# Kernel optimization log

Measured on AMD Instinct MI355X. Metric: run time of the kernel, lower is better.

Reference implementation:

```python
import math
import jax, jax.numpy as jnp
import numpy as np

N_HEADS = 8
N_POINTS = 4


def bilinear_sample(img, gx, gy):
    """torch F.grid_sample(bilinear, align_corners=True, padding='zeros').
    img: [N,C,H,W]; gx,gy: [N,P] normalized coords (gx -> width axis, gy -> height axis).
    Returns [N,C,P]."""
    N, C, H, W = img.shape
    ix = (gx + 1.0) * 0.5 * (W - 1)
    iy = (gy + 1.0) * 0.5 * (H - 1)
    x0 = jnp.floor(ix); y0 = jnp.floor(iy)
    x1 = x0 + 1.0;      y1 = y0 + 1.0

    def corner(yc, xc, w):
        m = (xc >= 0) & (xc <= W - 1) & (yc >= 0) & (yc <= H - 1)
        xi = jnp.clip(xc, 0, W - 1).astype(jnp.int32)
        yi = jnp.clip(yc, 0, H - 1).astype(jnp.int32)
        v = jax.vmap(lambda im, y, x: im[:, y, x])(img, yi, xi)  # [N,C,P]
        return v * (w * m)[:, None, :]

    return (corner(y0, x0, (x1 - ix) * (y1 - iy))
            + corner(y0, x1, (ix - x0) * (y1 - iy))
            + corner(y1, x0, (x1 - ix) * (iy - y0))
            + corner(y1, x1, (ix - x0) * (iy - y0)))


def forward(query, points, features, cam_M, cam_b, W_off, b_off,
            W_q, b_q, W_k, b_k, W_v, b_v, W_o, b_o):
    B, K, C = query.shape
    ncam = features.shape[0]
    H, W = features.shape[-2:]
    nh, npnt = N_HEADS, N_POINTS
    hd = C // nh
    HW = jnp.asarray([H, W], dtype=query.dtype)

    # camera model: pixel = sigmoid(points @ M^T + b) * [H, W]   -> [ncam,B,K,2]
    px = jax.nn.sigmoid(jnp.einsum('bkj,cij->cbki', points, cam_M)
                        + cam_b[:, None, None, :]) * HW

    # ---- step 1: sample raw features at projected points (per camera) ----
    # original normalizes coord0 by H and coord1 by W (coord0 is grid_sample's x/width axis)
    gx1 = 2.0 * px[..., 0] / H - 1.0          # [ncam,B,K]
    gy1 = 2.0 * px[..., 1] / W - 1.0
    camf = jax.vmap(bilinear_sample)(features, gx1, gy1)   # [ncam,B,C,K]
    camf = jnp.transpose(camf, (1, 3, 0, 2))               # [B,K,ncam,C]

    query_ = query[:, :, None, :] + camf                   # [B,K,ncam,C]
    offsets = (query_ @ W_off.T + b_off).reshape(B, K, ncam, nh, npnt, 2)

    # ---- 1x1 conv key/value projections ----
    kf = (jnp.einsum('cbdhw,ed->cbehw', features, W_k)
          + b_k[None, None, :, None, None]).reshape(ncam, B * nh, hd, H, W)
    vf = (jnp.einsum('cbdhw,ed->cbehw', features, W_v)
          + b_v[None, None, :, None, None]).reshape(ncam, B * nh, hd, H, W)

    # ---- sampling locations with offsets ----
    off = jnp.moveaxis(offsets, 2, 0) / HW                 # [ncam,B,K,nh,np,2]
    pc = px[:, :, :, None, None, :] + off                  # [ncam,B,K,nh,np,2]
    gx = 2.0 * (pc[..., 0] / H) - 1.0
    gy = 2.0 * (pc[..., 1] / W) - 1.0
    # [ncam,B,K,nh,np] -> [ncam, B*nh, K*np]
    gx = jnp.transpose(gx, (0, 1, 3, 2, 4)).reshape(ncam, B * nh, K * npnt)
    gy = jnp.transpose(gy, (0, 1, 3, 2, 4)).reshape(ncam, B * nh, K * npnt)

    keys = jax.vmap(bilinear_sample)(kf, gx, gy)           # [ncam,B*nh,hd,K*np]
    vals = jax.vmap(bilinear_sample)(vf, gx, gy)

    def rearr(t):  # -> [B, nh, K, ncam*np, hd]
        t = t.reshape(ncam, B, nh, hd, K, npnt)
        return jnp.transpose(t, (1, 2, 4, 0, 5, 3)).reshape(B, nh, K, ncam * npnt, hd)

    keys, vals = rearr(keys), rearr(vals)

    q = (query @ W_q.T + b_q).reshape(B, K, nh, hd).transpose(0, 2, 1, 3)  # [B,nh,K,hd]
    logits = jnp.einsum('bhkd,bhkld->bhkl', q, keys) / math.sqrt(hd)
    attn = jax.nn.softmax(logits, axis=-1)
    weighted = jnp.einsum('bhkl,bhkld->bhkd', attn, vals)  # [B,nh,K,hd]
    # faithful to original torch `.view(B, K, embed_dim)` on a [B,nh,K,hd] tensor
    weighted = weighted.reshape(B, K, C)
    return weighted @ W_o.T + b_o


def setup_inputs() -> dict:
    key = jax.random.key(0)
    ks = jax.random.split(key, 16)
    B, K, C = 8, 900, 256
    ncam, H, W = 6, 32, 88
    f = lambda i, shape, s=1.0: jax.random.normal(ks[i], shape, dtype=jnp.float32) * s
    return {
        'query': f(0, (B, K, C)),
        'points': f(1, (B, K, 3)),
        'features': f(2, (ncam, B, C, H, W)),
        'cam_M': f(3, (ncam, 2, 3), 0.5),
        'cam_b': f(4, (ncam, 2), 0.5),
        'W_off': f(5, (2 * N_HEADS * N_POINTS, C), 0.02),
        'b_off': f(6, (2 * N_HEADS * N_POINTS,), 1.0),
        'W_q': f(7, (C, C), 0.02), 'b_q': f(8, (C,), 0.02),
        'W_k': f(9, (C, C), 0.02), 'b_k': f(10, (C,), 0.02),
        'W_v': f(11, (C, C), 0.02), 'b_v': f(12, (C,), 0.02),
        'W_o': f(13, (C, C), 0.02), 'b_o': f(14, (C,), 0.02),
    }


def reference(query, points, features, cam_M, cam_b, W_off, b_off,
              W_q, b_q, W_k, b_k, W_v, b_v, W_o, b_o):
    return forward(query, points, features, cam_M, cam_b, W_off, b_off,
                   W_q, b_q, W_k, b_k, W_v, b_v, W_o, b_o)
```

## Files before the change

kernel.cpp:

```cpp
#include <hip/hip_runtime.h>

typedef __attribute__((ext_vector_type(4))) float f32x4;
typedef __attribute__((ext_vector_type(8))) short bf16x8;
typedef __attribute__((ext_vector_type(4))) unsigned int u32x4;

__device__ __forceinline__ unsigned short f2bf(float f) {
    union { float f; unsigned int u; } x; x.f = f;
    unsigned int u = x.u;
    return (unsigned short)((u + 0x7FFFu + ((u >> 16) & 1u)) >> 16);
}
__device__ __forceinline__ float bf2f(unsigned short b) {
    union { unsigned int u; float f; } x; x.u = ((unsigned int)b) << 16;
    return x.f;
}
__device__ __forceinline__ float u2f(unsigned int u) {
    union { unsigned int u; float f; } x; x.u = u; return x.f;
}


__global__ void prep_wkv(const float* __restrict__ Wk, const float* __restrict__ bk,
                         const float* __restrict__ Wv, const float* __restrict__ bv,
                         unsigned short* __restrict__ Wkv, float* __restrict__ bkv) {
    int i = blockIdx.x * 256 + threadIdx.x;
    if (i < 512 * 256) {
        int n = i >> 8, k = i & 255;
        float v = (n < 256) ? Wk[i] : Wv[i - 65536];
        Wkv[((size_t)(n >> 7) * 8 + (k >> 5)) * 4096 + (n & 127) * 32 + (k & 31)] = f2bf(v);
    }
    if (i < 512) bkv[i] = (i < 256) ? bk[i] : bv[i - 256];
}

__global__ void prep_woff(const float* __restrict__ Woff, unsigned short* __restrict__ Woffp) {
    int n = blockIdx.x, k = threadIdx.x;
    Woffp[(size_t)(k >> 5) * 4096 + n * 32 + (k & 31)] = f2bf(Woff[n * 256 + k]);
}

__global__ __launch_bounds__(256) void transpose_feat(const float* __restrict__ src,
                                                      unsigned short* __restrict__ dst) {
    __shared__ float tile[32][33];
    int img = blockIdx.z;
    int p0 = blockIdx.x * 32;
    int d0 = blockIdx.y * 32;
    int tx = threadIdx.x & 31, ty = threadIdx.x >> 5;
    const float* s = src + (size_t)img * 256 * 2816;
#pragma unroll
    for (int i = 0; i < 4; i++) tile[ty + 8 * i][tx] = s[(size_t)(d0 + ty + 8 * i) * 2816 + p0 + tx];
    __syncthreads();
    int m = img * 2816 + p0;
    unsigned short* o = dst + ((size_t)(m >> 7) * 8 + (d0 >> 5)) * 4096 + (m & 127) * 32;
#pragma unroll
    for (int i = 0; i < 4; i++) o[(ty + 8 * i) * 32 + tx] = f2bf(tile[tx][ty + 8 * i]);
}

__global__ __launch_bounds__(256) void gemm_kv2(
    const unsigned short* __restrict__ A,
    const unsigned short* __restrict__ Wkv,
    const unsigned short* __restrict__ Woffp,
    const float* __restrict__ bias,
    unsigned short* __restrict__ C,
    float* __restrict__ Foff) {
    __shared__ __align__(16) unsigned short Bl[8192];
    __shared__ __align__(16) unsigned short Ar[3][4096];

    const int tid = threadIdx.x, lane = tid & 63, w = tid >> 6;
    const int lrow = lane & 15, lk = lane >> 4;
    const int lsw = (lane >> 2) * 32 + (((lane & 3) ^ ((lane >> 3) & 3)) * 8);
    const int ckx = ((lrow >> 1) & 3);
    const int bid = blockIdx.x;
    const int wgid = (bid & 7) * 1188 + (bid >> 3);
    const int chunk = wgid / 9, bn = wgid % 9;

    const unsigned short* A0 = A + (size_t)chunk * 32768;
    const unsigned short* Bb = (bn < 8)
        ? Wkv + (size_t)(bn >> 1) * 32768 + (bn & 1) * 2048
        : Woffp;
    const int wof = w * 1024;

#define STAGE_B(HALF)                                                                        \
    {                                                                                        \
        _Pragma("unroll")                                                                    \
        for (int i = 0; i < 4; ++i) {                                                        \
            __builtin_amdgcn_global_load_lds(                                                \
                (const __attribute__((address_space(1))) unsigned int*)(Bb + ((HALF) * 4 + w) * 4096 + i * 512 + lsw), \
                (__attribute__((address_space(3))) unsigned int*)&Bl[w * 2048 + i * 512], 16, 0, 0);                   \
        }                                                                                    \
    }

#define STAGE_STEP(S)                                                                        \
    {                                                                                        \
        __builtin_amdgcn_global_load_lds(                                                    \
            (const __attribute__((address_space(1))) unsigned int*)(A0 + (S) * 4096 + wof + lsw),        \
            (__attribute__((address_space(3))) unsigned int*)&Ar[(S) % 3][wof], 16, 0, 0);   \
        __builtin_amdgcn_global_load_lds(                                                    \
            (const __attribute__((address_space(1))) unsigned int*)(A0 + (S) * 4096 + wof + 512 + lsw),  \
            (__attribute__((address_space(3))) unsigned int*)&Ar[(S) % 3][wof + 512], 16, 0, 0);         \
    }

    STAGE_B(0)
    STAGE_STEP(0) STAGE_STEP(1)
    __syncthreads();

    f32x4 acc[2][4] = {};

#define COMP_STEP(S, NW)                                                                     \
    {                                                                                        \
        asm volatile("s_waitcnt vmcnt(%0)" :: "i"(NW) : "memory");                           \
        bf16x8 bfr[4], af[2];                                                                \
        _Pragma("unroll") for (int j = 0; j < 4; ++j)                                        \
            bfr[j] = *(const bf16x8*)&Bl[((S) & 3) * 2048 + (j * 16 + lrow) * 32 + (lk ^ ckx) * 8]; \
        _Pragma("unroll") for (int i = 0; i < 2; ++i)                                        \
            af[i] = *(const bf16x8*)&Ar[(S) % 3][wof + i * 512 + lrow * 32 + (lk ^ ckx) * 8];\
        if ((S) + 2 < 8) {                                                                   \
            asm volatile("s_waitcnt lgkmcnt(0)" ::: "memory");                               \
            STAGE_STEP((S) + 2)                                                              \
        }                                                                                    \
        _Pragma("unroll") for (int i = 0; i < 2; ++i)                                        \
            _Pragma("unroll") for (int j = 0; j < 4; ++j)                                    \
                acc[i][j] = __builtin_amdgcn_mfma_f32_16x16x32_bf16(af[i], bfr[j], acc[i][j], 0, 0, 0); \
    }

    COMP_STEP(0, 4) COMP_STEP(1, 2) COMP_STEP(2, 2) COMP_STEP(3, 2)
    __syncthreads();
    STAGE_B(1)
    __syncthreads();
    COMP_STEP(4, 4) COMP_STEP(5, 2) COMP_STEP(6, 2) COMP_STEP(7, 0)
#undef COMP_STEP
#undef STAGE_STEP
#undef STAGE_B

    if (bn < 8) {
        unsigned short* Cl = &Ar[0][0];
        __syncthreads();
#pragma unroll
        for (int j = 0; j < 4; ++j) {
            float bs = bias[bn * 64 + j * 16 + lrow];
#pragma unroll
            for (int i = 0; i < 2; ++i)
#pragma unroll
                for (int jj = 0; jj < 4; ++jj)
                    Cl[(w * 32 + i * 16 + lk * 4 + jj) * 64 + j * 16 + lrow] =
                        f2bf(acc[i][j][jj] + bs);
        }
        __syncthreads();
#pragma unroll
        for (int it = 0; it < 4; ++it) {
            int idx = it * 256 + tid;
            int row = idx >> 3, col8 = idx & 7;
            int dstcol = (bn < 4)
                ? (bn * 2 + (col8 >> 2)) * 64 + (col8 & 3) * 8
                : ((bn - 4) * 2 + (col8 >> 2)) * 64 + 32 + (col8 & 3) * 8;
            *(f32x4*)(C + (size_t)(chunk * 128 + row) * 512 + dstcol) =
                *(const f32x4*)&Cl[row * 64 + col8 * 8];
        }
    } else {
#pragma unroll
        for (int i = 0; i < 2; ++i)
#pragma unroll
            for (int j = 0; j < 4; ++j)
#pragma unroll
                for (int jj = 0; jj < 4; ++jj) {
                    int m = chunk * 128 + w * 32 + i * 16 + lk * 4 + jj;
                    Foff[(size_t)m * 64 + j * 16 + lrow] = acc[i][j][jj];
                }
    }
}

__global__ __launch_bounds__(384) void sample_offs(
    const float* __restrict__ points, const float* __restrict__ camM,
    const float* __restrict__ camb, const float* __restrict__ Foff,
    const float* __restrict__ qWoff,
    float* __restrict__ offs, float* __restrict__ pxy) {
    int bk = blockIdx.x;
    int b = bk / 900;
    int cam = threadIdx.x >> 6, j = threadIdx.x & 63;
    int cid = cam * 7200 + bk;

    float p0 = points[(size_t)bk * 3 + 0];
    float p1 = points[(size_t)bk * 3 + 1];
    float p2 = points[(size_t)bk * 3 + 2];
    const float* M = camM + cam * 6;
    float s0 = M[0] * p0 + M[1] * p1 + M[2] * p2 + camb[cam * 2 + 0];
    float s1 = M[3] * p0 + M[4] * p1 + M[5] * p2 + camb[cam * 2 + 1];
    float px0 = (1.f / (1.f + expf(-s0))) * 32.f;
    float px1 = (1.f / (1.f + expf(-s1))) * 88.f;
    float gx = 2.f * px0 / 32.f - 1.f, gy = 2.f * px1 / 88.f - 1.f;
    float ix = (gx + 1.f) * 0.5f * 87.f;
    float iy = (gy + 1.f) * 0.5f * 31.f;
    float x0 = floorf(ix), y0 = floorf(iy), x1 = x0 + 1.f, y1 = y0 + 1.f;
    float wx1 = ix - x0, wx0 = x1 - ix, wy1 = iy - y0, wy0 = y1 - iy;
    float m00 = (x0 >= 0.f && x0 <= 87.f && y0 >= 0.f && y0 <= 31.f) ? 1.f : 0.f;
    float m01 = (x1 >= 0.f && x1 <= 87.f && y0 >= 0.f && y0 <= 31.f) ? 1.f : 0.f;
    float m10 = (x0 >= 0.f && x0 <= 87.f && y1 >= 0.f && y1 <= 31.f) ? 1.f : 0.f;
    float m11 = (x1 >= 0.f && x1 <= 87.f && y1 >= 0.f && y1 <= 31.f) ? 1.f : 0.f;
    float w00 = wx0 * wy0 * m00, w01 = wx1 * wy0 * m01, w10 = wx0 * wy1 * m10, w11 = wx1 * wy1 * m11;
    int xi0 = (int)fminf(fmaxf(x0, 0.f), 87.f);
    int xi1 = (int)fminf(fmaxf(x1, 0.f), 87.f);
    int yi0 = (int)fminf(fmaxf(y0, 0.f), 31.f);
    int yi1 = (int)fminf(fmaxf(y1, 0.f), 31.f);

    size_t base = (size_t)(cam * 8 + b) * 2816;
    const float* f00 = Foff + (base + yi0 * 88 + xi0) * 64;
    const float* f01 = Foff + (base + yi0 * 88 + xi1) * 64;
    const float* f10 = Foff + (base + yi1 * 88 + xi0) * 64;
    const float* f11 = Foff + (base + yi1 * 88 + xi1) * 64;

    float o = qWoff[(size_t)bk * 64 + j]
            + w00 * f00[j] + w01 * f01[j] + w10 * f10[j] + w11 * f11[j];
    offs[(size_t)cid * 64 + j] = o;
    if (j == 0) { pxy[cid * 2 + 0] = px0; pxy[cid * 2 + 1] = px1; }
}

template <bool SPLIT, bool C_BF16>
__global__ __launch_bounds__(256) void gemm_bf16(
    const float* __restrict__ A, long long aBatch,
    const float* __restrict__ B, const float* __restrict__ bias,
    void* __restrict__ Cv, long long cBatch,
    int M, int N, int K, int lda) {
    __shared__ __align__(16) unsigned short Ah[64][40];
    __shared__ __align__(16) unsigned short Bh[64][40];
    __shared__ __align__(16) unsigned short Al[(SPLIT ? 64 : 1)][40];
    __shared__ __align__(16) unsigned short Bl[(SPLIT ? 64 : 1)][40];

    const int tid = threadIdx.x;
    const int m0 = blockIdx.x * 64, n0 = blockIdx.y * 64;
    const int batch = blockIdx.z;
    const float* Ab = A + (size_t)batch * aBatch;
    const int lane = tid & 63, wave = tid >> 6;
    const int wr = wave & 1, wc = wave >> 1;
    const int lrow = lane & 15, lk = lane >> 4;

    f32x4 acc[2][2] = {};

    for (int kt = 0; kt < K; kt += 32) {
        if (kt) __syncthreads();
        {
            int c4 = (tid & 7) * 4;
#pragma unroll
            for (int rep = 0; rep < 2; rep++) {
                int r = (tid >> 3) + rep * 32;
                int m = m0 + r; if (m >= M) m = M - 1;
                f32x4 v = *(const f32x4*)(Ab + (size_t)m * lda + kt + c4);
#pragma unroll
                for (int q = 0; q < 4; q++) {
                    unsigned short h = f2bf(v[q]);
                    Ah[r][c4 + q] = h;
                    if (SPLIT) Al[r][c4 + q] = f2bf(v[q] - bf2f(h));
                }
            }
        }
        {
            int c4 = (tid & 7) * 4;
#pragma unroll
            for (int rep = 0; rep < 2; rep++) {
                int r = (tid >> 3) + rep * 32;
                f32x4 v = *(const f32x4*)(B + (size_t)(n0 + r) * K + kt + c4);
#pragma unroll
                for (int q = 0; q < 4; q++) {
                    unsigned short h = f2bf(v[q]);
                    Bh[r][c4 + q] = h;
                    if (SPLIT) Bl[r][c4 + q] = f2bf(v[q] - bf2f(h));
                }
            }
        }
        __syncthreads();

        bf16x8 a_h[2], b_h[2], a_l[2], b_l[2];
#pragma unroll
        for (int i = 0; i < 2; i++) {
            a_h[i] = *(const bf16x8*)&Ah[wr * 32 + i * 16 + lrow][lk * 8];
            b_h[i] = *(const bf16x8*)&Bh[wc * 32 + i * 16 + lrow][lk * 8];
            if (SPLIT) {
                a_l[i] = *(const bf16x8*)&Al[wr * 32 + i * 16 + lrow][lk * 8];
                b_l[i] = *(const bf16x8*)&Bl[wc * 32 + i * 16 + lrow][lk * 8];
            }
        }
#pragma unroll
        for (int i = 0; i < 2; i++)
#pragma unroll
            for (int j = 0; j < 2; j++) {
                acc[i][j] = __builtin_amdgcn_mfma_f32_16x16x32_bf16(a_h[i], b_h[j], acc[i][j], 0, 0, 0);
                if (SPLIT) {
                    acc[i][j] = __builtin_amdgcn_mfma_f32_16x16x32_bf16(a_h[i], b_l[j], acc[i][j], 0, 0, 0);
                    acc[i][j] = __builtin_amdgcn_mfma_f32_16x16x32_bf16(a_l[i], b_h[j], acc[i][j], 0, 0, 0);
                }
            }
    }

#pragma unroll
    for (int i = 0; i < 2; i++)
#pragma unroll
        for (int j = 0; j < 2; j++) {
            int n = n0 + wc * 32 + j * 16 + lrow;
            float bs = bias[n];
#pragma unroll
            for (int jj = 0; jj < 4; jj++) {
                int m = m0 + wr * 32 + i * 16 + lk * 4 + jj;
                if (m < M) {
                    float val = acc[i][j][jj] + bs;
                    if (C_BF16)
                        ((unsigned short*)Cv)[(size_t)batch * cBatch + (size_t)m * N + n] = f2bf(val);
                    else
                        ((float*)Cv)[(size_t)batch * cBatch + (size_t)m * N + n] = val;
                }
            }
        }
}

__global__ __launch_bounds__(512) void attn_kernel(
    const float* __restrict__ q_proj, const float* __restrict__ pxy,
    const float* __restrict__ offs, const unsigned short* __restrict__ kv_t,
    float* __restrict__ S) {
    int bk = blockIdx.x;
    int b = bk / 900, k = bk % 900;
    int h = threadIdx.x >> 6;
    int lane = threadIdx.x & 63;

    __shared__ __align__(16) float        ldsW[8][24][4];
    __shared__ __align__(16) unsigned int ldsI[8][24][4];
    __shared__ float ldsL[8][24];

    if (lane < 24) {
        int cam = lane >> 2, p = lane & 3;
        int cid = cam * 7200 + bk;
        float px0 = pxy[cid * 2 + 0], px1 = pxy[cid * 2 + 1];
        float o0 = offs[(size_t)cid * 64 + (h * 4 + p) * 2 + 0];
        float o1 = offs[(size_t)cid * 64 + (h * 4 + p) * 2 + 1];
        float pc0 = px0 + o0 * (1.f / 32.f);
        float pc1 = px1 + o1 * (1.f / 88.f);
        float gx = 2.f * (pc0 * (1.f / 32.f)) - 1.f;
        float gy = 2.f * (pc1 * (1.f / 88.f)) - 1.f;
        float ix = (gx + 1.f) * 0.5f * 87.f;
        float iy = (gy + 1.f) * 0.5f * 31.f;
        float x0 = floorf(ix), y0 = floorf(iy), x1 = x0 + 1.f, y1 = y0 + 1.f;
        float wx1 = ix - x0, wx0 = x1 - ix, wy1 = iy - y0, wy0 = y1 - iy;
        float m00 = (x0 >= 0.f && x0 <= 87.f && y0 >= 0.f && y0 <= 31.f) ? 1.f : 0.f;
        float m01 = (x1 >= 0.f && x1 <= 87.f && y0 >= 0.f && y0 <= 31.f) ? 1.f : 0.f;
        float m10 = (x0 >= 0.f && x0 <= 87.f && y1 >= 0.f && y1 <= 31.f) ? 1.f : 0.f;
        float m11 = (x1 >= 0.f && x1 <= 87.f && y1 >= 0.f && y1 <= 31.f) ? 1.f : 0.f;
        int xi0 = (int)fminf(fmaxf(x0, 0.f), 87.f);
        int xi1 = (int)fminf(fmaxf(x1, 0.f), 87.f);
        int yi0 = (int)fminf(fmaxf(y0, 0.f), 31.f);
        int yi1 = (int)fminf(fmaxf(y1, 0.f), 31.f);
        unsigned int img = (unsigned int)(cam * 8 + b) * 2816u;
        ldsW[h][lane][0] = wx0 * wy0 * m00;
        ldsW[h][lane][1] = wx1 * wy0 * m01;
        ldsW[h][lane][2] = wx0 * wy1 * m10;
        ldsW[h][lane][3] = wx1 * wy1 * m11;
        ldsI[h][lane][0] = (img + yi0 * 88 + xi0) * 1024u;
        ldsI[h][lane][1] = (img + yi0 * 88 + xi1) * 1024u;
        ldsI[h][lane][2] = (img + yi1 * 88 + xi0) * 1024u;
        ldsI[h][lane][3] = (img + yi1 * 88 + xi1) * 1024u;
    }
    __syncthreads();

    const int p8 = lane >> 3, dlane = lane & 7;
    const int chB = h * 128 + dlane * 16;
    const char* kvb = (const char*)kv_t;

    f32x4 qa = *(const f32x4*)(q_proj + (size_t)bk * 256 + h * 32 + (dlane & 3) * 8);
    f32x4 qb = *(const f32x4*)(q_proj + (size_t)bk * 256 + h * 32 + (dlane & 3) * 8 + 4);

    float vr[3][8];
    const float inv_sqrt = 0.17677669529663687f;
#pragma unroll
    for (int it = 0; it < 3; ++it) {
        int l = it * 8 + p8;
        f32x4 w = *(const f32x4*)ldsW[h][l];
        unsigned int i0 = ldsI[h][l][0], i1 = ldsI[h][l][1];
        unsigned int i2 = ldsI[h][l][2], i3 = ldsI[h][l][3];
        u32x4 u0 = *(const u32x4*)(kvb + i0 + chB);
        u32x4 u1 = *(const u32x4*)(kvb + i1 + chB);
        u32x4 u2 = *(const u32x4*)(kvb + i2 + chB);
        u32x4 u3 = *(const u32x4*)(kvb + i3 + chB);
#pragma unroll
        for (int q = 0; q < 4; ++q) {
            vr[it][2 * q] = w[0] * u2f(u0[q] << 16) + w[1] * u2f(u1[q] << 16)
                          + w[2] * u2f(u2[q] << 16) + w[3] * u2f(u3[q] << 16);
            vr[it][2 * q + 1] = w[0] * u2f(u0[q] & 0xFFFF0000u) + w[1] * u2f(u1[q] & 0xFFFF0000u)
                              + w[2] * u2f(u2[q] & 0xFFFF0000u) + w[3] * u2f(u3[q] & 0xFFFF0000u);
        }
        float t = qa[0] * vr[it][0] + qa[1] * vr[it][1] + qa[2] * vr[it][2] + qa[3] * vr[it][3]
                + qb[0] * vr[it][4] + qb[1] * vr[it][5] + qb[2] * vr[it][6] + qb[3] * vr[it][7];
        t += __shfl_xor(t, 1);
        t += __shfl_xor(t, 2);
        if (dlane == 0) ldsL[h][l] = t * inv_sqrt;
    }
    __syncthreads();

    float mx = -1e30f;
#pragma unroll
    for (int l = 0; l < 24; l++) mx = fmaxf(mx, ldsL[h][l]);
    float ssum = 0.f;
    float at3[3];
#pragma unroll
    for (int l = 0; l < 24; l++) {
        float e = __expf(ldsL[h][l] - mx);
        ssum += e;
        if ((l & 7) == p8) at3[l >> 3] = e;
    }
    float inv = 1.f / ssum;

    float o[8];
#pragma unroll
    for (int j = 0; j < 8; ++j)
        o[j] = at3[0] * vr[0][j] + at3[1] * vr[1][j] + at3[2] * vr[2][j];
#pragma unroll
    for (int j = 0; j < 8; ++j) {
        o[j] += __shfl_xor(o[j], 8);
        o[j] += __shfl_xor(o[j], 16);
        o[j] += __shfl_xor(o[j], 32);
    }
    if (p8 == 0 && dlane >= 4) {
        int d0 = (dlane - 4) * 8;
        f32x4 v0, v1;
        v0[0] = o[0] * inv; v0[1] = o[1] * inv; v0[2] = o[2] * inv; v0[3] = o[3] * inv;
        v1[0] = o[4] * inv; v1[1] = o[5] * inv; v1[2] = o[6] * inv; v1[3] = o[7] * inv;
        float* dst = &S[(size_t)b * 230400 + (size_t)h * 28800 + k * 32 + d0];
        *(f32x4*)dst = v0;
        *(f32x4*)(dst + 4) = v1;
    }
}

extern "C" void kernel_launch(void* const* d_in, const int* in_sizes, int n_in,
                              void* d_out, int out_size, void* d_ws, size_t ws_size,
                              hipStream_t stream) {
    const float* query    = (const float*)d_in[0];
    const float* points   = (const float*)d_in[1];
    const float* features = (const float*)d_in[2];
    const float* camM     = (const float*)d_in[3];
    const float* camb     = (const float*)d_in[4];
    const float* W_off    = (const float*)d_in[5];
    const float* b_off    = (const float*)d_in[6];
    const float* W_q      = (const float*)d_in[7];
    const float* b_q      = (const float*)d_in[8];
    const float* W_k      = (const float*)d_in[9];
    const float* b_k      = (const float*)d_in[10];
    const float* W_v      = (const float*)d_in[11];
    const float* b_v      = (const float*)d_in[12];
    const float* W_o      = (const float*)d_in[13];
    const float* b_o      = (const float*)d_in[14];

    char* ws = (char*)d_ws;
    unsigned short* feat_t = (unsigned short*)ws; ws += 69206016;
    unsigned short* kv_t   = (unsigned short*)ws; ws += 138412032;
    float* Foff   = (float*)ws; ws += 34603008;
    float* offs   = (float*)ws; ws += 11059200;
    float* pxy    = (float*)ws; ws += 345600;
    float* qWoff  = (float*)ws; ws += 1843200;
    float* q_proj = (float*)ws; ws += 7372800;
    float* S      = (float*)ws; ws += 7372800;
    unsigned short* Wkv = (unsigned short*)ws; ws += 524288;
    float* bkv    = (float*)ws; ws += 2048;
    unsigned short* Woffp = (unsigned short*)ws; ws += 65536;

    prep_wkv<<<512, 256, 0, stream>>>(W_k, b_k, W_v, b_v, Wkv, bkv);
    prep_woff<<<64, 256, 0, stream>>>(W_off, Woffp);
    transpose_feat<<<dim3(88, 8, 48), 256, 0, stream>>>(features, feat_t);
    gemm_kv2<<<9504, 256, 0, stream>>>(feat_t, Wkv, Woffp, bkv, kv_t, Foff);
    gemm_bf16<true, false><<<dim3(113, 1, 1), 256, 0, stream>>>(
        query, 0, W_off, b_off, qWoff, 0, 7200, 64, 256, 256);
    sample_offs<<<7200, 384, 0, stream>>>(points, camM, camb, Foff, qWoff, offs, pxy);
    gemm_bf16<true, false><<<dim3(113, 4, 1), 256, 0, stream>>>(
        query, 0, W_q, b_q, q_proj, 0, 7200, 256, 256, 256);
    attn_kernel<<<7200, 512, 0, stream>>>(q_proj, pxy, offs, kv_t, S);
    gemm_bf16<true, false><<<dim3(113, 4, 1), 256, 0, stream>>>(
        S, 0, W_o, b_o, d_out, 0, 7200, 256, 256, 256);
}
```

Baseline: 255.3 us.

## Double GEMM M-tile to 256 rows and preload full B panel once

The kv/offset GEMM now has each workgroup compute 256 rows instead of 128, with each wave holding a 64x64 accumulator block, which halves the grid. The whole 64-column weight panel for all K steps is loaded into LDS up front, replacing the two-half B staging and its mid-loop barriers. This is meant to halve redundant weight traffic per output row and remove synchronization. In exchange LDS use roughly doubles and register pressure rises, which may lower occupancy, and the epilogue is split into two serialized passes through LDS.

Result: no change. 259.7 us (+1.7%).

```diff
diff --git a/kernel.cpp b/kernel.cpp
--- a/kernel.cpp
+++ b/kernel.cpp
@@ -59,107 +59,106 @@
     const float* __restrict__ bias,
     unsigned short* __restrict__ C,
     float* __restrict__ Foff) {
-    __shared__ __align__(16) unsigned short Bl[8192];
-    __shared__ __align__(16) unsigned short Ar[3][4096];
+    __shared__ __align__(16) unsigned short Bl[16384];
+    __shared__ __align__(16) unsigned short Ar[3][8192];
 
     const int tid = threadIdx.x, lane = tid & 63, w = tid >> 6;
     const int lrow = lane & 15, lk = lane >> 4;
     const int lsw = (lane >> 2) * 32 + (((lane & 3) ^ ((lane >> 3) & 3)) * 8);
     const int ckx = ((lrow >> 1) & 3);
     const int bid = blockIdx.x;
-    const int wgid = (bid & 7) * 1188 + (bid >> 3);
+    const int wgid = (bid & 7) * 594 + (bid >> 3);
     const int chunk = wgid / 9, bn = wgid % 9;
 
-    const unsigned short* A0 = A + (size_t)chunk * 32768;
+    const unsigned short* A0 = A + (size_t)chunk * 65536;
     const unsigned short* Bb = (bn < 8)
         ? Wkv + (size_t)(bn >> 1) * 32768 + (bn & 1) * 2048
         : Woffp;
-    const int wof = w * 1024;
-
-#define STAGE_B(HALF)                                                                        \
+    const int wsrc = (w >> 1) * 32768 + (w & 1) * 2048;
+    const int wdst = w * 2048;
+
+#pragma unroll
+    for (int i = 0; i < 8; ++i) {
+        int kt = w * 2 + (i >> 2), part = i & 3;
+        __builtin_amdgcn_global_load_lds(
+            (const __attribute__((address_space(1))) unsigned int*)(Bb + kt * 4096 + part * 512 + lsw),
+            (__attribute__((address_space(3))) unsigned int*)&Bl[kt * 2048 + part * 512], 16, 0, 0);
+    }
+
+#define STAGE_STEP(S)                                                                        \
     {                                                                                        \
         _Pragma("unroll")                                                                    \
         for (int i = 0; i < 4; ++i) {                                                        \
             __builtin_amdgcn_global_load_lds(                                                \
-                (const __attribute__((address_space(1))) unsigned int*)(Bb + ((HALF) * 4 + w) * 4096 + i * 512 + lsw), \
-                (__attribute__((address_space(3))) unsigned int*)&Bl[w * 2048 + i * 512], 16, 0, 0);                   \
+                (const __attribute__((address_space(1))) unsigned int*)(A0 + wsrc + (S) * 4096 + i * 512 + lsw), \
+                (__attribute__((address_space(3))) unsigned int*)&Ar[(S) % 3][wdst + i * 512], 16, 0, 0);        \
         }                                                                                    \
     }
 
-#define STAGE_STEP(S)                                                                        \
-    {                                                                                        \
-        __builtin_amdgcn_global_load_lds(                                                    \
-            (const __attribute__((address_space(1))) unsigned int*)(A0 + (S) * 4096 + wof + lsw),        \
-            (__attribute__((address_space(3))) unsigned int*)&Ar[(S) % 3][wof], 16, 0, 0);   \
-        __builtin_amdgcn_global_load_lds(                                                    \
-            (const __attribute__((address_space(1))) unsigned int*)(A0 + (S) * 4096 + wof + 512 + lsw),  \
-            (__attribute__((address_space(3))) unsigned int*)&Ar[(S) % 3][wof + 512], 16, 0, 0);         \
-    }
-
-    STAGE_B(0)
     STAGE_STEP(0) STAGE_STEP(1)
     __syncthreads();
 
-    f32x4 acc[2][4] = {};
+    f32x4 acc[4][4] = {};
 
 #define COMP_STEP(S, NW)                                                                     \
     {                                                                                        \
         asm volatile("s_waitcnt vmcnt(%0)" :: "i"(NW) : "memory");                           \
-        bf16x8 bfr[4], af[2];                                                                \
+        bf16x8 bfr[4], af[4];                                                                \
         _Pragma("unroll") for (int j = 0; j < 4; ++j)                                        \
-            bfr[j] = *(const bf16x8*)&Bl[((S) & 3) * 2048 + (j * 16 + lrow) * 32 + (lk ^ ckx) * 8]; \
-        _Pragma("unroll") for (int i = 0; i < 2; ++i)                                        \
-            af[i] = *(const bf16x8*)&Ar[(S) % 3][wof + i * 512 + lrow * 32 + (lk ^ ckx) * 8];\
+            bfr[j] = *(const bf16x8*)&Bl[(S) * 2048 + (j * 16 + lrow) * 32 + (lk ^ ckx) * 8];\
+        _Pragma("unroll") for (int i = 0; i < 4; ++i)                                        \
+            af[i] = *(const bf16x8*)&Ar[(S) % 3][wdst + (i * 16 + lrow) * 32 + (lk ^ ckx) * 8]; \
         if ((S) + 2 < 8) {                                                                   \
             asm volatile("s_waitcnt lgkmcnt(0)" ::: "memory");                               \
             STAGE_STEP((S) + 2)                                                              \
         }                                                                                    \
-        _Pragma("unroll") for (int i = 0; i < 2; ++i)                                        \
+        _Pragma("unroll") for (int i = 0; i < 4; ++i)                                        \
             _Pragma("unroll") for (int j = 0; j < 4; ++j)                                    \
                 acc[i][j] = __builtin_amdgcn_mfma_f32_16x16x32_bf16(af[i], bfr[j], acc[i][j], 0, 0, 0); \
     }
 
-    COMP_STEP(0, 4) COMP_STEP(1, 2) COMP_STEP(2, 2) COMP_STEP(3, 2)
-    __syncthreads();
-    STAGE_B(1)
-    __syncthreads();
-    COMP_STEP(4, 4) COMP_STEP(5, 2) COMP_STEP(6, 2) COMP_STEP(7, 0)
+    COMP_STEP(0, 63) COMP_STEP(1, 63) COMP_STEP(2, 4) COMP_STEP(3, 4)
+    COMP_STEP(4, 4)  COMP_STEP(5, 4)  COMP_STEP(6, 4) COMP_STEP(7, 0)
 #undef COMP_STEP
 #undef STAGE_STEP
-#undef STAGE_B
 
     if (bn < 8) {
         unsigned short* Cl = &Ar[0][0];
-        __syncthreads();
-#pragma unroll
-        for (int j = 0; j < 4; ++j) {
-            float bs = bias[bn * 64 + j * 16 + lrow];
-#pragma unroll
-            for (int i = 0; i < 2; ++i)
-#pragma unroll
-                for (int jj = 0; jj < 4; ++jj)
-                    Cl[(w * 32 + i * 16 + lk * 4 + jj) * 64 + j * 16 + lrow] =
-                        f2bf(acc[i][j][jj] + bs);
-        }
-        __syncthreads();
-#pragma unroll
-        for (int it = 0; it < 4; ++it) {
-            int idx = it * 256 + tid;
-            int row = idx >> 3, col8 = idx & 7;
-            int dstcol = (bn < 4)
-                ? (bn * 2 + (col8 >> 2)) * 64 + (col8 & 3) * 8
-                : ((bn - 4) * 2 + (col8 >> 2)) * 64 + 32 + (col8 & 3) * 8;
-            *(f32x4*)(C + (size_t)(chunk * 128 + row) * 512 + dstcol) =
-                *(const f32x4*)&Cl[row * 64 + col8 * 8];
+#pragma unroll
+        for (int p = 0; p < 2; ++p) {
+            __syncthreads();
+            if ((w >> 1) == p) {
+#pragma unroll
+                for (int j = 0; j < 4; ++j) {
+                    float bs = bias[bn * 64 + j * 16 + lrow];
+#pragma unroll
+                    for (int i = 0; i < 4; ++i)
+#pragma unroll
+                        for (int jj = 0; jj < 4; ++jj)
+                            Cl[((w & 1) * 64 + i * 16 + lk * 4 + jj) * 64 + j * 16 + lrow] =
+                                f2bf(acc[i][j][jj] + bs);
+                }
+            }
+            __syncthreads();
+#pragma unroll
+            for (int it = 0; it < 4; ++it) {
+                int idx = it * 256 + tid;
+                int row = idx >> 3, col8 = idx & 7;
+                int dstcol = (bn < 4)
+                    ? (bn * 2 + (col8 >> 2)) * 64 + (col8 & 3) * 8
+                    : ((bn - 4) * 2 + (col8 >> 2)) * 64 + 32 + (col8 & 3) * 8;
+                *(f32x4*)(C + (size_t)(chunk * 256 + p * 128 + row) * 512 + dstcol) =
+                    *(const f32x4*)&Cl[row * 64 + col8 * 8];
+            }
         }
     } else {
 #pragma unroll
-        for (int i = 0; i < 2; ++i)
+        for (int i = 0; i < 4; ++i)
 #pragma unroll
             for (int j = 0; j < 4; ++j)
 #pragma unroll
                 for (int jj = 0; jj < 4; ++jj) {
-                    int m = chunk * 128 + w * 32 + i * 16 + lk * 4 + jj;
+                    int m = chunk * 256 + w * 64 + i * 16 + lk * 4 + jj;
                     Foff[(size_t)m * 64 + j * 16 + lrow] = acc[i][j][jj];
                 }
     }
@@ -456,7 +455,7 @@
     prep_wkv<<<512, 256, 0, stream>>>(W_k, b_k, W_v, b_v, Wkv, bkv);
     prep_woff<<<64, 256, 0, stream>>>(W_off, Woffp);
     transpose_feat<<<dim3(88, 8, 48), 256, 0, stream>>>(features, feat_t);
-    gemm_kv2<<<9504, 256, 0, stream>>>(feat_t, Wkv, Woffp, bkv, kv_t, Foff);
+    gemm_kv2<<<4752, 256, 0, stream>>>(feat_t, Wkv, Woffp, bkv, kv_t, Foff);
     gemm_bf16<true, false><<<dim3(113, 1, 1), 256, 0, stream>>>(
         query, 0, W_off, b_off, qWoff, 0, 7200, 64, 256, 256);
     sample_offs<<<7200, 384, 0, stream>>>(points, camM, camb, Foff, qWoff, offs, pxy);
```

## Stage full B tile once, deepen A pipeline, and merge q/offset projections

Applied to the files above, without the earlier changes.

The feature GEMM now loads the whole 256-deep weight tile into shared memory at the start and keeps a 4-deep A ring buffer with 3 steps in flight. This removes the mid-loop barriers and the B reload, and drops the lgkmcnt wait before issuing new loads. The query projection and the query-offset projection are fused into a single 320-wide GEMM with concatenated weights, and the two prep kernels are merged into one launch. The larger LDS footprint may limit occupancy, and launch_bounds now requests 2 blocks.

Result: faster. 246.0 us (-3.6%).

```diff
diff --git a/kernel.cpp b/kernel.cpp
--- a/kernel.cpp
+++ b/kernel.cpp
@@ -18,9 +18,13 @@
 }
 
 
-__global__ void prep_wkv(const float* __restrict__ Wk, const float* __restrict__ bk,
+__global__ void prep_all(const float* __restrict__ Wk, const float* __restrict__ bk,
                          const float* __restrict__ Wv, const float* __restrict__ bv,
-                         unsigned short* __restrict__ Wkv, float* __restrict__ bkv) {
+                         const float* __restrict__ Wq, const float* __restrict__ bq,
+                         const float* __restrict__ Woff, const float* __restrict__ boff,
+                         unsigned short* __restrict__ Wkv, float* __restrict__ bkv,
+                         unsigned short* __restrict__ Woffp,
+                         float* __restrict__ Wcat, float* __restrict__ bcat) {
     int i = blockIdx.x * 256 + threadIdx.x;
     if (i < 512 * 256) {
         int n = i >> 8, k = i & 255;
@@ -28,11 +32,12 @@
         Wkv[((size_t)(n >> 7) * 8 + (k >> 5)) * 4096 + (n & 127) * 32 + (k & 31)] = f2bf(v);
     }
     if (i < 512) bkv[i] = (i < 256) ? bk[i] : bv[i - 256];
-}
-
-__global__ void prep_woff(const float* __restrict__ Woff, unsigned short* __restrict__ Woffp) {
-    int n = blockIdx.x, k = threadIdx.x;
-    Woffp[(size_t)(k >> 5) * 4096 + n * 32 + (k & 31)] = f2bf(Woff[n * 256 + k]);
+    if (i < 64 * 256) {
+        int n = i >> 8, k = i & 255;
+        Woffp[(size_t)(k >> 5) * 4096 + n * 32 + (k & 31)] = f2bf(Woff[i]);
+    }
+    if (i < 320 * 256) Wcat[i] = (i < 65536) ? Wq[i] : Woff[i - 65536];
+    if (i < 320) bcat[i] = (i < 256) ? bq[i] : boff[i - 256];
 }
 
 __global__ __launch_bounds__(256) void transpose_feat(const float* __restrict__ src,
@@ -52,15 +57,15 @@
     for (int i = 0; i < 4; i++) o[(ty + 8 * i) * 32 + tx] = f2bf(tile[tx][ty + 8 * i]);
 }
 
-__global__ __launch_bounds__(256) void gemm_kv2(
+__global__ __launch_bounds__(256, 2) void gemm_kv2(
     const unsigned short* __restrict__ A,
     const unsigned short* __restrict__ Wkv,
     const unsigned short* __restrict__ Woffp,
     const float* __restrict__ bias,
     unsigned short* __restrict__ C,
     float* __restrict__ Foff) {
-    __shared__ __align__(16) unsigned short Bl[8192];
-    __shared__ __align__(16) unsigned short Ar[3][4096];
+    __shared__ __align__(16) unsigned short Bl[16384];
+    __shared__ __align__(16) unsigned short Ar[4][4096];
 
     const int tid = threadIdx.x, lane = tid & 63, w = tid >> 6;
     const int lrow = lane & 15, lk = lane >> 4;
@@ -76,28 +81,25 @@
         : Woffp;
     const int wof = w * 1024;
 
-#define STAGE_B(HALF)                                                                        \
-    {                                                                                        \
-        _Pragma("unroll")                                                                    \
-        for (int i = 0; i < 4; ++i) {                                                        \
-            __builtin_amdgcn_global_load_lds(                                                \
-                (const __attribute__((address_space(1))) unsigned int*)(Bb + ((HALF) * 4 + w) * 4096 + i * 512 + lsw), \
-                (__attribute__((address_space(3))) unsigned int*)&Bl[w * 2048 + i * 512], 16, 0, 0);                   \
-        }                                                                                    \
+#pragma unroll
+    for (int i = 0; i < 8; ++i) {
+        int kt = w * 2 + (i >> 2), part = i & 3;
+        __builtin_amdgcn_global_load_lds(
+            (const __attribute__((address_space(1))) unsigned int*)(Bb + kt * 4096 + part * 512 + lsw),
+            (__attribute__((address_space(3))) unsigned int*)&Bl[kt * 2048 + part * 512], 16, 0, 0);
     }
 
 #define STAGE_STEP(S)                                                                        \
     {                                                                                        \
         __builtin_amdgcn_global_load_lds(                                                    \
             (const __attribute__((address_space(1))) unsigned int*)(A0 + (S) * 4096 + wof + lsw),        \
-            (__attribute__((address_space(3))) unsigned int*)&Ar[(S) % 3][wof], 16, 0, 0);   \
+            (__attribute__((address_space(3))) unsigned int*)&Ar[(S) & 3][wof], 16, 0, 0);   \
         __builtin_amdgcn_global_load_lds(                                                    \
             (const __attribute__((address_space(1))) unsigned int*)(A0 + (S) * 4096 + wof + 512 + lsw),  \
-            (__attribute__((address_space(3))) unsigned int*)&Ar[(S) % 3][wof + 512], 16, 0, 0);         \
-    }
-
-    STAGE_B(0)
-    STAGE_STEP(0) STAGE_STEP(1)
+            (__attribute__((address_space(3))) unsigned int*)&Ar[(S) & 3][wof + 512], 16, 0, 0);         \
+    }
+
+    STAGE_STEP(0) STAGE_STEP(1) STAGE_STEP(2)
     __syncthreads();
 
     f32x4 acc[2][4] = {};
@@ -107,26 +109,19 @@
         asm volatile("s_waitcnt vmcnt(%0)" :: "i"(NW) : "memory");                           \
         bf16x8 bfr[4], af[2];                                                                \
         _Pragma("unroll") for (int j = 0; j < 4; ++j)                                        \
-            bfr[j] = *(const bf16x8*)&Bl[((S) & 3) * 2048 + (j * 16 + lrow) * 32 + (lk ^ ckx) * 8]; \
+            bfr[j] = *(const bf16x8*)&Bl[(S) * 2048 + (j * 16 + lrow) * 32 + (lk ^ ckx) * 8];\
         _Pragma("unroll") for (int i = 0; i < 2; ++i)                                        \
-            af[i] = *(const bf16x8*)&Ar[(S) % 3][wof + i * 512 + lrow * 32 + (lk ^ ckx) * 8];\
-        if ((S) + 2 < 8) {                                                                   \
-            asm volatile("s_waitcnt lgkmcnt(0)" ::: "memory");                               \
-            STAGE_STEP((S) + 2)                                                              \
-        }                                                                                    \
+            af[i] = *(const bf16x8*)&Ar[(S) & 3][wof + i * 512 + lrow * 32 + (lk ^ ckx) * 8];\
+        if ((S) + 3 < 8) STAGE_STEP((S) + 3)                                                 \
         _Pragma("unroll") for (int i = 0; i < 2; ++i)                                        \
             _Pragma("unroll") for (int j = 0; j < 4; ++j)                                    \
                 acc[i][j] = __builtin_amdgcn_mfma_f32_16x16x32_bf16(af[i], bfr[j], acc[i][j], 0, 0, 0); \
     }
 
-    COMP_STEP(0, 4) COMP_STEP(1, 2) COMP_STEP(2, 2) COMP_STEP(3, 2)
-    __syncthreads();
-    STAGE_B(1)
-    __syncthreads();
-    COMP_STEP(4, 4) COMP_STEP(5, 2) COMP_STEP(6, 2) COMP_STEP(7, 0)
+    COMP_STEP(0, 63) COMP_STEP(1, 63) COMP_STEP(2, 63) COMP_STEP(3, 4)
+    COMP_STEP(4, 4)  COMP_STEP(5, 4)  COMP_STEP(6, 2)  COMP_STEP(7, 0)
 #undef COMP_STEP
 #undef STAGE_STEP
-#undef STAGE_B
 
     if (bn < 8) {
         unsigned short* Cl = &Ar[0][0];
@@ -168,7 +163,7 @@
 __global__ __launch_bounds__(384) void sample_offs(
     const float* __restrict__ points, const float* __restrict__ camM,
     const float* __restrict__ camb, const float* __restrict__ Foff,
-    const float* __restrict__ qWoff,
+    const float* __restrict__ qcat,
     float* __restrict__ offs, float* __restrict__ pxy) {
     int bk = blockIdx.x;
     int b = bk / 900;
@@ -204,7 +199,7 @@
     const float* f10 = Foff + (base + yi1 * 88 + xi0) * 64;
     const float* f11 = Foff + (base + yi1 * 88 + xi1) * 64;
 
-    float o = qWoff[(size_t)bk * 64 + j]
+    float o = qcat[(size_t)bk * 320 + 256 + j]
             + w00 * f00[j] + w01 * f01[j] + w10 * f10[j] + w11 * f11[j];
     offs[(size_t)cid * 64 + j] = o;
     if (j == 0) { pxy[cid * 2 + 0] = px0; pxy[cid * 2 + 1] = px1; }
@@ -307,7 +302,7 @@
 }
 
 __global__ __launch_bounds__(512) void attn_kernel(
-    const float* __restrict__ q_proj, const float* __restrict__ pxy,
+    const float* __restrict__ qcat, const float* __restrict__ pxy,
     const float* __restrict__ offs, const unsigned short* __restrict__ kv_t,
     float* __restrict__ S) {
     int bk = blockIdx.x;
@@ -357,8 +352,8 @@
     const int chB = h * 128 + dlane * 16;
     const char* kvb = (const char*)kv_t;
 
-    f32x4 qa = *(const f32x4*)(q_proj + (size_t)bk * 256 + h * 32 + (dlane & 3) * 8);
-    f32x4 qb = *(const f32x4*)(q_proj + (size_t)bk * 256 + h * 32 + (dlane & 3) * 8 + 4);
+    f32x4 qa = *(const f32x4*)(qcat + (size_t)bk * 320 + h * 32 + (dlane & 3) * 8);
+    f32x4 qb = *(const f32x4*)(qcat + (size_t)bk * 320 + h * 32 + (dlane & 3) * 8 + 4);
 
     float vr[3][8];
     const float inv_sqrt = 0.17677669529663687f;
@@ -446,23 +441,22 @@
     float* Foff   = (float*)ws; ws += 34603008;
     float* offs   = (float*)ws; ws += 11059200;
     float* pxy    = (float*)ws; ws += 345600;
-    float* qWoff  = (float*)ws; ws += 1843200;
-    float* q_proj = (float*)ws; ws += 7372800;
+    float* qcat   = (float*)ws; ws += 9216000;
     float* S      = (float*)ws; ws += 7372800;
     unsigned short* Wkv = (unsigned short*)ws; ws += 524288;
     float* bkv    = (float*)ws; ws += 2048;
     unsigned short* Woffp = (unsigned short*)ws; ws += 65536;
-
-    prep_wkv<<<512, 256, 0, stream>>>(W_k, b_k, W_v, b_v, Wkv, bkv);
-    prep_woff<<<64, 256, 0, stream>>>(W_off, Woffp);
+    float* Wcat   = (float*)ws; ws += 327680;
+    float* bcat   = (float*)ws; ws += 1280;
+
+    prep_all<<<512, 256, 0, stream>>>(W_k, b_k, W_v, b_v, W_q, b_q, W_off, b_off,
+                                      Wkv, bkv, Woffp, Wcat, bcat);
     transpose_feat<<<dim3(88, 8, 48), 256, 0, stream>>>(features, feat_t);
     gemm_kv2<<<9504, 256, 0, stream>>>(feat_t, Wkv, Woffp, bkv, kv_t, Foff);
-    gemm_bf16<true, false><<<dim3(113, 1, 1), 256, 0, stream>>>(
-        query, 0, W_off, b_off, qWoff, 0, 7200, 64, 256, 256);
-    sample_offs<<<7200, 384, 0, stream>>>(points, camM, camb, Foff, qWoff, offs, pxy);
-    gemm_bf16<true, false><<<dim3(113, 4, 1), 256, 0, stream>>>(
-        query, 0, W_q, b_q, q_proj, 0, 7200, 256, 256, 256);
-    attn_kernel<<<7200, 512, 0, stream>>>(q_proj, pxy, offs, kv_t, S);
+    gemm_bf16<true, false><<<dim3(113, 5, 1), 256, 0, stream>>>(
+        query, 0, Wcat, bcat, qcat, 0, 7200, 320, 256, 256);
+    sample_offs<<<7200, 384, 0, stream>>>(points, camM, camb, Foff, qcat, offs, pxy);
+    attn_kernel<<<7200, 512, 0, stream>>>(qcat, pxy, offs, kv_t, S);
     gemm_bf16<true, false><<<dim3(113, 4, 1), 256, 0, stream>>>(
         S, 0, W_o, b_o, d_out, 0, 7200, 256, 256, 256);
 }
```
